# Optimization experiments

Measured on AMD Instinct MI355X. Metric: run time of the kernel, lower is better.

Reference implementation:

```python
import jax, jax.numpy as jnp
import numpy as np

B, S, D, H = 4, 2048, 1024, 16
HD = D // H  # head_size = 64
SCALE = HD ** -0.5


def setup_inputs() -> dict:
    key = jax.random.key(0)
    k1, k2, k3 = jax.random.split(key, 3)
    hidden_states = jax.random.normal(k1, (B, S, D), dtype=jnp.float32)
    W_qkv = jax.random.normal(k2, (D, 3 * D), dtype=jnp.float32) * 0.02
    W_out = jax.random.normal(k3, (D, D), dtype=jnp.float32) * 0.02
    return {"hidden_states": hidden_states, "W_qkv": W_qkv, "W_out": W_out}


def reference(hidden_states, W_qkv, W_out):
    b, s, d = hidden_states.shape
    qkv = hidden_states @ W_qkv                      # [b, s, 3d]
    q, k, v = jnp.split(qkv, 3, axis=-1)
    # [b, s, d] -> [b, H, s, hd]
    q = q.reshape(b, s, H, HD).transpose(0, 2, 1, 3)
    k = k.reshape(b, s, H, HD).transpose(0, 2, 1, 3)
    v = v.reshape(b, s, H, HD).transpose(0, 2, 1, 3)
    scores = jnp.einsum("bhqd,bhkd->bhqk", q, k) * SCALE  # [b, H, s, s]
    probs = jax.nn.softmax(scores, axis=-1)
    ctx = jnp.einsum("bhqk,bhkd->bhqd", probs, v)         # [b, H, s, hd]
    ctx = ctx.transpose(0, 2, 1, 3).reshape(b, s, d)
    out = ctx @ W_out
    return out
```

## Files before the change

kernel.cpp:

```cpp
#include <hip/hip_runtime.h>

typedef __attribute__((ext_vector_type(8))) __bf16 bf8;
typedef __attribute__((ext_vector_type(4))) float f4;
typedef __attribute__((ext_vector_type(8))) unsigned short us8;
typedef __attribute__((ext_vector_type(4))) unsigned short us4;
typedef __attribute__((ext_vector_type(4))) unsigned int u32x4;
typedef __attribute__((ext_vector_type(2))) unsigned int u32x2;

#define MFMA16(a, b, c) __builtin_amdgcn_mfma_f32_16x16x32_bf16((a), (b), (c), 0, 0, 0)
#define GLOAD16(gp, lp)                                                        \
  __builtin_amdgcn_global_load_lds(                                            \
      (const __attribute__((address_space(1))) void*)(gp),                     \
      (__attribute__((address_space(3))) void*)(lp), 16, 0, 0)

__device__ __forceinline__ unsigned short f2bf(float f) {
  unsigned u = __builtin_bit_cast(unsigned, f);
  u += 0x7FFFu + ((u >> 16) & 1u);
  return (unsigned short)(u >> 16);
}

__device__ __forceinline__ float fexp2(float x) {
  float r;
  asm("v_exp_f32 %0, %1" : "=v"(r) : "v"(x));
  return r;
}

__device__ __forceinline__ unsigned cvtpk(float a, float b) {
  unsigned r;
  asm("v_cvt_pk_bf16_f32 %0, %1, %2" : "=v"(r) : "v"(a), "v"(b));
  return r;
}

__global__ __launch_bounds__(256) void c_cast(const float* __restrict__ in,
                                              unsigned short* __restrict__ out) {
  int i = blockIdx.x * 256 + threadIdx.x;
  const float4* p = reinterpret_cast<const float4*>(in) + (size_t)i * 2;
  float4 a = p[0], b = p[1];
  us8 o;
  o[0] = f2bf(a.x); o[1] = f2bf(a.y); o[2] = f2bf(a.z); o[3] = f2bf(a.w);
  o[4] = f2bf(b.x); o[5] = f2bf(b.y); o[6] = f2bf(b.z); o[7] = f2bf(b.w);
  *reinterpret_cast<us8*>(&out[(size_t)i * 8]) = o;
}

__global__ __launch_bounds__(256) void c_trans(const float* __restrict__ in,
                                               unsigned short* __restrict__ out,
                                               int R, int C) {
  __shared__ float T[64][65];
  const int t = threadIdx.x;
  const int c0 = blockIdx.x * 64, r0 = blockIdx.y * 64;
  const int tr = t >> 4, tc = (t & 15) * 4;
#pragma unroll
  for (int i = 0; i < 4; ++i) {
    int r = tr + i * 16;
    float4 v = *reinterpret_cast<const float4*>(&in[(size_t)(r0 + r) * C + c0 + tc]);
    T[r][tc] = v.x; T[r][tc + 1] = v.y; T[r][tc + 2] = v.z; T[r][tc + 3] = v.w;
  }
  __syncthreads();
#pragma unroll
  for (int i = 0; i < 4; ++i) {
    int c = tr + i * 16;
    us4 o;
    o[0] = f2bf(T[tc + 0][c]); o[1] = f2bf(T[tc + 1][c]);
    o[2] = f2bf(T[tc + 2][c]); o[3] = f2bf(T[tc + 3][c]);
    *reinterpret_cast<us4*>(&out[(size_t)(c0 + c) * R + r0 + tc]) = o;
  }
}

__global__ __launch_bounds__(256) void k_qkv(const unsigned short* __restrict__ A,
                                             const unsigned short* __restrict__ Bt,
                                             unsigned short* __restrict__ Qo,
                                             unsigned short* __restrict__ Ko,
                                             unsigned short* __restrict__ Vo) {
  __shared__ unsigned short As[2][128 * 32];
  __shared__ unsigned short Bs[2][128 * 32];
  const int t = threadIdx.x;
  const int lane = t & 63, wid = t >> 6;
  const int wr = wid >> 1, wc = wid & 1;
  const int cl = lane & 15, kr8 = (lane >> 4) << 3;
  const int m0 = blockIdx.x << 7, n0 = blockIdx.y << 7;

  f4 acc[4][4];
#pragma unroll
  for (int i = 0; i < 4; ++i)
#pragma unroll
    for (int j = 0; j < 4; ++j) acc[i][j] = (f4){0.f, 0.f, 0.f, 0.f};

  auto STAGE = [&](int buf, int kt) {
    int k0 = kt << 5;
#pragma unroll
    for (int it = 0; it < 2; ++it) {
      int c = t + (it << 8);
      int wb = (t & 192) + (it << 8);
      GLOAD16(A + (size_t)(m0 + (c >> 2)) * 1024 + k0 + ((c & 3) << 3),
              (char*)As[buf] + (size_t)wb * 16);
      GLOAD16(Bt + (size_t)(n0 + (c >> 2)) * 1024 + k0 + ((c & 3) << 3),
              (char*)Bs[buf] + (size_t)wb * 16);
    }
  };

  STAGE(0, 0);
  __syncthreads();
  for (int kt = 0; kt < 32; ++kt) {
    int cur = kt & 1;
    if (kt < 31) STAGE(cur ^ 1, kt + 1);
    const unsigned short* as = As[cur];
    const unsigned short* bs = Bs[cur];
    bf8 af[4], bfr[4];
#pragma unroll
    for (int mi = 0; mi < 4; ++mi)
      af[mi] = *reinterpret_cast<const bf8*>(&as[(wr * 64 + mi * 16 + cl) * 32 + kr8]);
#pragma unroll
    for (int ni = 0; ni < 4; ++ni)
      bfr[ni] = *reinterpret_cast<const bf8*>(&bs[(wc * 64 + ni * 16 + cl) * 32 + kr8]);
#pragma unroll
    for (int mi = 0; mi < 4; ++mi)
#pragma unroll
      for (int ni = 0; ni < 4; ++ni)
        acc[mi][ni] = MFMA16(af[mi], bfr[ni], acc[mi][ni]);
    __syncthreads();
  }

#pragma unroll
  for (int mi = 0; mi < 4; ++mi) {
#pragma unroll
    for (int ni = 0; ni < 4; ++ni) {
      int gcol = n0 + wc * 64 + ni * 16 + cl;
      int grow0 = m0 + wr * 64 + mi * 16 + ((lane >> 4) << 2);
      int b = grow0 >> 11, s0 = grow0 & 2047;
      if (gcol < 1024) {
        int h = gcol >> 6, hd = gcol & 63;
#pragma unroll
        for (int r = 0; r < 4; ++r)
          Qo[((size_t)(b * 16 + h) * 2048 + s0 + r) * 64 + hd] =
              f2bf(acc[mi][ni][r] * 0.18033688011112042f);
      } else if (gcol < 2048) {
        int cc = gcol - 1024;
        int h = cc >> 6, hd = cc & 63;
#pragma unroll
        for (int r = 0; r < 4; ++r)
          Ko[((size_t)(b * 16 + h) * 2048 + s0 + r) * 64 + hd] = f2bf(acc[mi][ni][r]);
      } else {
        int cc = gcol - 2048;
        int h = cc >> 6, hd = cc & 63;
        us4 o;
        o[0] = f2bf(acc[mi][ni][0]); o[1] = f2bf(acc[mi][ni][1]);
        o[2] = f2bf(acc[mi][ni][2]); o[3] = f2bf(acc[mi][ni][3]);
        *reinterpret_cast<us4*>(&Vo[((size_t)(b * 16 + h) * 64 + hd) * 2048 + s0]) = o;
      }
    }
  }
}

__global__ __launch_bounds__(512) void k_attn(const unsigned short* __restrict__ Q,
                                              const unsigned short* __restrict__ K,
                                              const unsigned short* __restrict__ Vt,
                                              unsigned short* __restrict__ Ctx) {
  __shared__ __align__(16) unsigned short SMEM[2][2][64 * 64];
  __shared__ float RedS[128];
  const int t = threadIdx.x;
  const int lane = t & 63, wid = t >> 6;
  const int cl = lane & 15, g = lane >> 4;
  const int qg = wid >> 1, kg = wid & 1;
  const int bh = blockIdx.y, b = bh >> 4, h = bh & 15;
  const int q0 = blockIdx.x << 7;
  const size_t base = (size_t)bh * (2048 * 64);

  bf8 qf[2][2];
#pragma unroll
  for (int qi = 0; qi < 2; ++qi) {
    int qrow = q0 + qg * 32 + qi * 16 + cl;
    qf[qi][0] = *reinterpret_cast<const bf8*>(&Q[base + (size_t)qrow * 64 + (g << 3)]);
    qf[qi][1] = *reinterpret_cast<const bf8*>(&Q[base + (size_t)qrow * 64 + 32 + (g << 3)]);
  }

  const unsigned ones_u = 0x3F803F80u;
  u32x4 ones4 = (u32x4){ones_u, ones_u, ones_u, ones_u};
  bf8 onesb = __builtin_bit_cast(bf8, ones4);
  const f4 minit = (f4){-12.f, -12.f, -12.f, -12.f};

  f4 o[2][4], osum[2];
#pragma unroll
  for (int qi = 0; qi < 2; ++qi) {
#pragma unroll
    for (int n = 0; n < 4; ++n) o[qi][n] = (f4){0.f, 0.f, 0.f, 0.f};
    osum[qi] = (f4){0.f, 0.f, 0.f, 0.f};
  }

  auto STAGEK = [&](int buf, int kv0) {
    int kvl = t >> 3;
    int dblk = (t & 7) ^ (kvl & 7);
    GLOAD16(K + base + (size_t)(kv0 + kvl) * 64 + (dblk << 3),
            (char*)SMEM[0][buf] + (size_t)(t & 448) * 16);
  };
  auto STAGEV = [&](int buf, int kv0) {
    int d = t >> 3, ch = t & 7;
    int kq = ch ^ ((d >> 1) & 7);
    GLOAD16(Vt + base + (size_t)d * 2048 + kv0 + (kq << 3),
            (char*)SMEM[1][buf] + (size_t)(t & 448) * 16);
  };

  STAGEK(0, 0);
  STAGEV(0, 0);
  __syncthreads();

  for (int tk = 0; tk < 32; ++tk) {
    int cur = tk & 1;
    if (tk < 31) {
      STAGEK(cur ^ 1, (tk + 1) << 6);
      STAGEV(cur ^ 1, (tk + 1) << 6);
    }
    const char* kp = (const char*)SMEM[0][cur];
    const char* vp = (const char*)SMEM[1][cur];

    f4 sT[2][2];
    __builtin_amdgcn_s_setprio(1);
#pragma unroll
    for (int cb = 0; cb < 2; ++cb) {
      int row = (2 * kg + cb) * 16 + cl;
      bf8 a0 = *reinterpret_cast<const bf8*>(kp + row * 128 + ((g ^ (cl & 7)) << 4));
      bf8 a1 = *reinterpret_cast<const bf8*>(kp + row * 128 + (((4 + g) ^ (cl & 7)) << 4));
#pragma unroll
      for (int qi = 0; qi < 2; ++qi) {
        f4 s = minit;
        s = MFMA16(a0, qf[qi][0], s);
        s = MFMA16(a1, qf[qi][1], s);
        sT[cb][qi] = s;
      }
    }
    __builtin_amdgcn_s_setprio(0);

    u32x4 pw[2];
#pragma unroll
    for (int qi = 0; qi < 2; ++qi) {
      pw[qi][0] = cvtpk(fexp2(sT[0][qi][0]), fexp2(sT[0][qi][1]));
      pw[qi][1] = cvtpk(fexp2(sT[0][qi][2]), fexp2(sT[0][qi][3]));
      pw[qi][2] = cvtpk(fexp2(sT[1][qi][0]), fexp2(sT[1][qi][1]));
      pw[qi][3] = cvtpk(fexp2(sT[1][qi][2]), fexp2(sT[1][qi][3]));
    }
    bf8 pa0 = __builtin_bit_cast(bf8, pw[0]);
    bf8 pa1 = __builtin_bit_cast(bf8, pw[1]);

    const int q1 = 8 * kg + g, q2 = 8 * kg + 4 + g;
    unsigned vb = (unsigned)(cl * 128);
    unsigned o1 = (unsigned)((q1 ^ (cl & 14)) << 3);
    unsigned o2 = (unsigned)((q2 ^ (cl & 14)) << 3);
    __builtin_amdgcn_s_setprio(1);
#pragma unroll
    for (int n = 0; n < 4; ++n) {
      unsigned a = vb + (unsigned)(n * 2048);
      u32x2 lo = *reinterpret_cast<const u32x2*>(vp + a + o1);
      u32x2 hi = *reinterpret_cast<const u32x2*>(vp + a + o2);
      u32x4 bw = (u32x4){lo[0], lo[1], hi[0], hi[1]};
      bf8 vb8 = __builtin_bit_cast(bf8, bw);
      o[0][n] = MFMA16(pa0, vb8, o[0][n]);
      o[1][n] = MFMA16(pa1, vb8, o[1][n]);
    }
    osum[0] = MFMA16(pa0, onesb, osum[0]);
    osum[1] = MFMA16(pa1, onesb, osum[1]);
    __builtin_amdgcn_s_setprio(0);

    __syncthreads();
  }

  float* red = (float*)SMEM;
  if (kg) {
#pragma unroll
    for (int qi = 0; qi < 2; ++qi) {
#pragma unroll
      for (int n = 0; n < 4; ++n) {
        int ridx = qg * 8 + qi * 4 + n;
        *reinterpret_cast<f4*>(red + ridx * 256 + cl * 16 + g * 4) = o[qi][n];
      }
      if (cl == 0)
        *reinterpret_cast<f4*>(&RedS[(qg * 2 + qi) * 16 + g * 4]) = osum[qi];
    }
  }
  __syncthreads();
  if (!kg) {
#pragma unroll
    for (int qi = 0; qi < 2; ++qi) {
#pragma unroll
      for (int n = 0; n < 4; ++n) {
        int ridx = qg * 8 + qi * 4 + n;
        f4 po = *reinterpret_cast<const f4*>(red + ridx * 256 + cl * 16 + g * 4);
        o[qi][n] += po;
      }
      f4 ps = *reinterpret_cast<const f4*>(&RedS[(qg * 2 + qi) * 16 + g * 4]);
      osum[qi] += ps;
#pragma unroll
      for (int r = 0; r < 4; ++r) {
        float inv = 1.0f / osum[qi][r];
        int s = q0 + qg * 32 + qi * 16 + (g << 2) + r;
        size_t rb = ((size_t)b * 2048 + s) * 1024 + h * 64;
#pragma unroll
        for (int n = 0; n < 4; ++n) Ctx[rb + n * 16 + cl] = f2bf(o[qi][n][r] * inv);
      }
    }
  }
}

__global__ __launch_bounds__(256) void k_oproj(const unsigned short* __restrict__ A,
                                               const unsigned short* __restrict__ Bt,
                                               float* __restrict__ Out) {
  __shared__ unsigned short As[2][128 * 32];
  __shared__ unsigned short Bs[2][128 * 32];
  const int t = threadIdx.x;
  const int lane = t & 63, wid = t >> 6;
  const int wr = wid >> 1, wc = wid & 1;
  const int cl = lane & 15, kr8 = (lane >> 4) << 3;
  const int m0 = blockIdx.x << 7, n0 = blockIdx.y << 7;

  f4 acc[4][4];
#pragma unroll
  for (int i = 0; i < 4; ++i)
#pragma unroll
    for (int j = 0; j < 4; ++j) acc[i][j] = (f4){0.f, 0.f, 0.f, 0.f};

  auto STAGE = [&](int buf, int kt) {
    int k0 = kt << 5;
#pragma unroll
    for (int it = 0; it < 2; ++it) {
      int c = t + (it << 8);
      int wb = (t & 192) + (it << 8);
      GLOAD16(A + (size_t)(m0 + (c >> 2)) * 1024 + k0 + ((c & 3) << 3),
              (char*)As[buf] + (size_t)wb * 16);
      GLOAD16(Bt + (size_t)(n0 + (c >> 2)) * 1024 + k0 + ((c & 3) << 3),
              (char*)Bs[buf] + (size_t)wb * 16);
    }
  };

  STAGE(0, 0);
  __syncthreads();
  for (int kt = 0; kt < 32; ++kt) {
    int cur = kt & 1;
    if (kt < 31) STAGE(cur ^ 1, kt + 1);
    const unsigned short* as = As[cur];
    const unsigned short* bs = Bs[cur];
    bf8 af[4], bfr[4];
#pragma unroll
    for (int mi = 0; mi < 4; ++mi)
      af[mi] = *reinterpret_cast<const bf8*>(&as[(wr * 64 + mi * 16 + cl) * 32 + kr8]);
#pragma unroll
    for (int ni = 0; ni < 4; ++ni)
      bfr[ni] = *reinterpret_cast<const bf8*>(&bs[(wc * 64 + ni * 16 + cl) * 32 + kr8]);
#pragma unroll
    for (int mi = 0; mi < 4; ++mi)
#pragma unroll
      for (int ni = 0; ni < 4; ++ni)
        acc[mi][ni] = MFMA16(af[mi], bfr[ni], acc[mi][ni]);
    __syncthreads();
  }

#pragma unroll
  for (int mi = 0; mi < 4; ++mi) {
#pragma unroll
    for (int ni = 0; ni < 4; ++ni) {
      int gcol = n0 + wc * 64 + ni * 16 + cl;
#pragma unroll
      for (int r = 0; r < 4; ++r) {
        int grow = m0 + wr * 64 + mi * 16 + ((lane >> 4) << 2) + r;
        Out[(size_t)grow * 1024 + gcol] = acc[mi][ni][r];
      }
    }
  }
}

extern "C" void kernel_launch(void* const* d_in, const int* in_sizes, int n_in,
                              void* d_out, int out_size, void* d_ws, size_t ws_size,
                              hipStream_t stream) {
  const float* hs = (const float*)d_in[0];
  const float* wqkv = (const float*)d_in[1];
  const float* wout = (const float*)d_in[2];
  float* out = (float*)d_out;

  unsigned short* ws = (unsigned short*)d_ws;
  const size_t NHS = (size_t)8192 * 1024;
  const size_t NWQ = (size_t)1024 * 3072;
  const size_t NWO = (size_t)1024 * 1024;
  const size_t NQ = (size_t)64 * 2048 * 64;

  unsigned short* hsb = ws;
  unsigned short* wqt = ws + NHS;
  unsigned short* wot = wqt + NWQ;
  unsigned short* Qw = wot + NWO;
  unsigned short* Kw = Qw + NQ;
  unsigned short* Vw = Kw + NQ;
  unsigned short* Cw = hsb;

  c_cast<<<dim3(4096), 256, 0, stream>>>(hs, hsb);
  c_trans<<<dim3(48, 16), 256, 0, stream>>>(wqkv, wqt, 1024, 3072);
  c_trans<<<dim3(16, 16), 256, 0, stream>>>(wout, wot, 1024, 1024);
  k_qkv<<<dim3(64, 24), 256, 0, stream>>>(hsb, wqt, Qw, Kw, Vw);
  k_attn<<<dim3(16, 64), 512, 0, stream>>>(Qw, Kw, Vw, Cw);
  k_oproj<<<dim3(64, 8), 256, 0, stream>>>(Cw, wot, out);
}
```

Before: 197.4 us.

## Swizzle block order for XCD locality and shrink attention block to 64 queries

```diff
diff --git a/kernel.cpp b/kernel.cpp
--- a/kernel.cpp
+++ b/kernel.cpp
@@ -77,7 +77,9 @@
   const int lane = t & 63, wid = t >> 6;
   const int wr = wid >> 1, wc = wid & 1;
   const int cl = lane & 15, kr8 = (lane >> 4) << 3;
-  const int m0 = blockIdx.x << 7, n0 = blockIdx.y << 7;
+  const int id = blockIdx.x;
+  const int s = (id & 7) * 192 + (id >> 3);
+  const int m0 = (s / 24) << 7, n0 = (s % 24) << 7;
 
   f4 acc[4][4];
 #pragma unroll
@@ -151,18 +153,22 @@
   }
 }
 
-__global__ __launch_bounds__(512) void k_attn(const unsigned short* __restrict__ Q,
+__global__ __launch_bounds__(256) void k_attn(const unsigned short* __restrict__ Q,
                                               const unsigned short* __restrict__ K,
                                               const unsigned short* __restrict__ Vt,
                                               unsigned short* __restrict__ Ctx) {
-  __shared__ __align__(16) unsigned short SMEM[2][2][64 * 64];
+  __shared__ __align__(16) unsigned short Ks[2][64 * 64];
+  __shared__ __align__(16) unsigned short Vs[64 * 64];
   __shared__ float RedS[128];
   const int t = threadIdx.x;
   const int lane = t & 63, wid = t >> 6;
   const int cl = lane & 15, g = lane >> 4;
   const int qg = wid >> 1, kg = wid & 1;
-  const int bh = blockIdx.y, b = bh >> 4, h = bh & 15;
-  const int q0 = blockIdx.x << 7;
+  const int id = blockIdx.x;
+  const int sw = (id & 7) * 256 + (id >> 3);
+  const int bh = sw >> 5, qb = sw & 31;
+  const int b = bh >> 4, h = bh & 15;
+  const int q0 = qb << 6;
   const size_t base = (size_t)bh * (2048 * 64);
 
   bf8 qf[2][2];
@@ -187,30 +193,46 @@
   }
 
   auto STAGEK = [&](int buf, int kv0) {
-    int kvl = t >> 3;
-    int dblk = (t & 7) ^ (kvl & 7);
-    GLOAD16(K + base + (size_t)(kv0 + kvl) * 64 + (dblk << 3),
-            (char*)SMEM[0][buf] + (size_t)(t & 448) * 16);
+#pragma unroll
+    for (int it = 0; it < 2; ++it) {
+      int c = t + (it << 8);
+      int kvl = c >> 3;
+      int dblk = (c & 7) ^ (kvl & 7);
+      GLOAD16(K + base + (size_t)(kv0 + kvl) * 64 + (dblk << 3),
+              (char*)Ks[buf] + (size_t)((t & 192) + (it << 8)) * 16);
+    }
   };
-  auto STAGEV = [&](int buf, int kv0) {
-    int d = t >> 3, ch = t & 7;
-    int kq = ch ^ ((d >> 1) & 7);
-    GLOAD16(Vt + base + (size_t)d * 2048 + kv0 + (kq << 3),
-            (char*)SMEM[1][buf] + (size_t)(t & 448) * 16);
+  auto VLOAD = [&](u32x4 vr[2], int kv0) {
+#pragma unroll
+    for (int it = 0; it < 2; ++it) {
+      int c = t + (it << 8);
+      int d = c >> 3;
+      int kq = (c & 7) ^ ((d >> 1) & 7);
+      vr[it] = *reinterpret_cast<const u32x4*>(Vt + base + (size_t)d * 2048 + kv0 + (kq << 3));
+    }
   };
-
+  auto VWRITE = [&](const u32x4 vr[2]) {
+#pragma unroll
+    for (int it = 0; it < 2; ++it) {
+      int c = t + (it << 8);
+      *reinterpret_cast<u32x4*>((char*)Vs + (size_t)c * 16) = vr[it];
+    }
+  };
+
+  u32x4 vr[2];
+  VLOAD(vr, 0);
   STAGEK(0, 0);
-  STAGEV(0, 0);
+  VWRITE(vr);
   __syncthreads();
 
   for (int tk = 0; tk < 32; ++tk) {
     int cur = tk & 1;
     if (tk < 31) {
       STAGEK(cur ^ 1, (tk + 1) << 6);
-      STAGEV(cur ^ 1, (tk + 1) << 6);
-    }
-    const char* kp = (const char*)SMEM[0][cur];
-    const char* vp = (const char*)SMEM[1][cur];
+      VLOAD(vr, (tk + 1) << 6);
+    }
+    const char* kp = (const char*)Ks[cur];
+    const char* vp = (const char*)Vs;
 
     f4 sT[2][2];
     __builtin_amdgcn_s_setprio(1);
@@ -260,9 +282,13 @@
     __builtin_amdgcn_s_setprio(0);
 
     __syncthreads();
-  }
-
-  float* red = (float*)SMEM;
+    if (tk < 31) {
+      VWRITE(vr);
+      __syncthreads();
+    }
+  }
+
+  float* red = (float*)Ks;
   if (kg) {
 #pragma unroll
     for (int qi = 0; qi < 2; ++qi) {
@@ -308,7 +334,9 @@
   const int lane = t & 63, wid = t >> 6;
   const int wr = wid >> 1, wc = wid & 1;
   const int cl = lane & 15, kr8 = (lane >> 4) << 3;
-  const int m0 = blockIdx.x << 7, n0 = blockIdx.y << 7;
+  const int id = blockIdx.x;
+  const int s = (id & 7) * 64 + (id >> 3);
+  const int m0 = (s >> 3) << 7, n0 = (s & 7) << 7;
 
   f4 acc[4][4];
 #pragma unroll
@@ -390,7 +418,7 @@
   c_cast<<<dim3(4096), 256, 0, stream>>>(hs, hsb);
   c_trans<<<dim3(48, 16), 256, 0, stream>>>(wqkv, wqt, 1024, 3072);
   c_trans<<<dim3(16, 16), 256, 0, stream>>>(wout, wot, 1024, 1024);
-  k_qkv<<<dim3(64, 24), 256, 0, stream>>>(hsb, wqt, Qw, Kw, Vw);
-  k_attn<<<dim3(16, 64), 512, 0, stream>>>(Qw, Kw, Vw, Cw);
-  k_oproj<<<dim3(64, 8), 256, 0, stream>>>(Cw, wot, out);
-}
+  k_qkv<<<dim3(1536), 256, 0, stream>>>(hsb, wqt, Qw, Kw, Vw);
+  k_attn<<<dim3(2048), 256, 0, stream>>>(Qw, Kw, Vw, Cw);
+  k_oproj<<<dim3(512), 256, 0, stream>>>(Cw, wot, out);
+}
```

Result: slower. 231.8 us (+17.4%).
